# Kernel optimization log

Hardware: AMD Instinct MI355X
Metric: run time of the kernel (lower is better)

Reference implementation:

```python
import jax, jax.numpy as jnp
import numpy as np


def _ln(x, w, b):
    m = x.mean(-1, keepdims=True)
    v = x.var(-1, keepdims=True)
    return (x - m) * jax.lax.rsqrt(v + 1e-5) * w + b


def setup_inputs() -> dict:
    key = jax.random.key(0)
    ks = jax.random.split(key, 12)
    B, Cm, T, D, H = 8, 192, 2048, 512, 1536
    n_fft, hop = 1024, 256
    nF = n_fft // 2 + 1
    s = 0.05
    rn = lambda k, shape: jax.random.normal(k, shape, jnp.float32) * s
    window = (0.5 - 0.5 * jnp.cos(2.0 * jnp.pi * jnp.arange(n_fft, dtype=jnp.float32) / n_fft))
    return dict(
        mel=jax.random.normal(ks[0], (B, Cm, T), jnp.float32),
        embed_w=rn(ks[1], (D, Cm, 7)), embed_b=rn(ks[2], (D,)),
        norm_w=jnp.ones((D,), jnp.float32), norm_b=jnp.zeros((D,), jnp.float32),
        blk_dw_w=rn(ks[3], (8, D, 1, 7)), blk_dw_b=rn(ks[4], (8, D)),
        blk_norm_w=jnp.ones((8, D), jnp.float32), blk_norm_b=jnp.zeros((8, D), jnp.float32),
        blk_pw1_w=rn(ks[5], (8, H, D)), blk_pw1_b=rn(ks[6], (8, H)),
        blk_pw2_w=rn(ks[7], (8, D, H)), blk_pw2_b=rn(ks[8], (8, D)),
        blk_gamma=jnp.full((8, D), 0.1, jnp.float32),
        fnorm_w=jnp.ones((D,), jnp.float32), fnorm_b=jnp.zeros((D,), jnp.float32),
        head_w=rn(ks[9], (2 * nF, D)), head_b=rn(ks[10], (2 * nF,)),
        window=window,
        n_fft=n_fft, hop_length=hop,
    )


def _vocoder(mel, embed_w, embed_b, norm_w, norm_b,
             blk_dw_w, blk_dw_b, blk_norm_w, blk_norm_b,
             blk_pw1_w, blk_pw1_b, blk_pw2_w, blk_pw2_b, blk_gamma,
             fnorm_w, fnorm_b, head_w, head_b, window, n_fft, hop_length):
    D = embed_w.shape[0]
    # embed conv: [B,192,T] -> [B,512,T]
    x = jax.lax.conv_general_dilated(mel, embed_w, (1,), [(3, 3)],
                                     dimension_numbers=('NCH', 'OIH', 'NCH'))
    x = x + embed_b[None, :, None]
    x = _ln(x.transpose(0, 2, 1), norm_w, norm_b).transpose(0, 2, 1)

    def blk(x, p):
        dw, db, nw, nb, w1, b1, w2, b2, g = p
        y = jax.lax.conv_general_dilated(x, dw, (1,), [(3, 3)],
                                         dimension_numbers=('NCH', 'OIH', 'NCH'),
                                         feature_group_count=D)
        y = y + db[None, :, None]
        y = _ln(y.transpose(0, 2, 1), nw, nb)          # [B,T,D]
        y = jax.nn.gelu(jnp.einsum('btc,hc->bth', y, w1) + b1, approximate=False)
        y = jnp.einsum('bth,ch->btc', y, w2) + b2
        return x + (g * y).transpose(0, 2, 1), None

    x, _ = jax.lax.scan(blk, x, (blk_dw_w, blk_dw_b, blk_norm_w, blk_norm_b,
                                 blk_pw1_w, blk_pw1_b, blk_pw2_w, blk_pw2_b, blk_gamma))

    h = _ln(x.transpose(0, 2, 1), fnorm_w, fnorm_b)    # [B,T,D]
    out = jnp.einsum('btc,fc->btf', h, head_w) + head_b  # [B,T,2*nF]
    nF = n_fft // 2 + 1
    mag = jnp.minimum(jnp.exp(out[..., :nF]), 100.0)   # [B,T,nF]
    phase = out[..., nF:]
    S_real = mag * jnp.cos(phase)
    S_imag = mag * jnp.sin(phase)

    # real inverse-DFT basis
    n = jnp.arange(n_fft, dtype=jnp.float32)
    k = jnp.arange(nF, dtype=jnp.float32)
    ang = 2.0 * jnp.pi * n[:, None] * k[None, :] / n_fft
    scale = jnp.full((nF,), 2.0 / n_fft, jnp.float32)
    scale = scale.at[0].set(1.0 / n_fft)
    if n_fft % 2 == 0:
        scale = scale.at[-1].set(1.0 / n_fft)
    cos_b = jnp.cos(ang) * scale[None, :]              # [n_fft, nF]
    sin_b = jnp.sin(ang) * scale[None, :]

    frames = (jnp.einsum('btf,nf->btn', S_real, cos_b)
              - jnp.einsum('btf,nf->btn', S_imag, sin_b))  # [B,T,n_fft]
    frames = frames * window[None, None, :]

    B, T, N = frames.shape
    L = (T - 1) * hop_length + n_fft
    idx = jnp.arange(T)[:, None] * hop_length + jnp.arange(n_fft)[None, :]  # [T,n_fft]
    audio = jnp.zeros((B, L), frames.dtype).at[:, idx].add(frames)
    win_sq = window * window
    win_env = jnp.zeros((L,), frames.dtype).at[idx].add(
        jnp.broadcast_to(win_sq, (T, n_fft)))
    audio = audio / (win_env[None, :] + 1e-11)
    c = n_fft // 2
    return audio[:, c:-c]


def reference(mel, embed_w, embed_b, norm_w, norm_b,
              blk_dw_w, blk_dw_b, blk_norm_w, blk_norm_b,
              blk_pw1_w, blk_pw1_b, blk_pw2_w, blk_pw2_b, blk_gamma,
              fnorm_w, fnorm_b, head_w, head_b, window, n_fft, hop_length):
    return _vocoder(mel, embed_w, embed_b, norm_w, norm_b,
                    blk_dw_w, blk_dw_b, blk_norm_w, blk_norm_b,
                    blk_pw1_w, blk_pw1_b, blk_pw2_w, blk_pw2_b, blk_gamma,
                    fnorm_w, fnorm_b, head_w, head_b, window, n_fft, hop_length)
```

## Files before the change

### kernel.cpp

```cpp
#include <hip/hip_runtime.h>
#include <cmath>

#define B_ 8
#define T_ 2048
#define BT_ 16384
#define D_ 512
#define H_ 1536
#define CM_ 192
#define KE_ 1344
#define TP_ 2054
#define NFFT_ 1024
#define NF_ 513
#define HOP_ 256
#define NO2_ 1026
#define NPAD_ 1152
#define KI_ 1088
#define LOUT_ 524032

typedef _Float16 f16;
typedef f16 f16x8 __attribute__((ext_vector_type(8)));
typedef float f32x4 __attribute__((ext_vector_type(4)));

__device__ __forceinline__ float gelu_f(float v) {
    float u = 0.7978845608028654f * v * (1.0f + 0.044715f * v * v);
    float e = __expf(2.0f * u);
    float t = 1.0f - 2.0f * __builtin_amdgcn_rcpf(e + 1.0f);
    return 0.5f * v * (1.0f + t);
}

__device__ __forceinline__ void gload16(const void* g, void* s) {
    __builtin_amdgcn_global_load_lds((const __attribute__((address_space(1))) void*)g,
                                     (__attribute__((address_space(3))) void*)s, 16, 0, 0);
}


__global__ __launch_bounds__(256) void k_cvt(const float* __restrict__ src,
                                             f16* __restrict__ dst, int n) {
    int i = blockIdx.x * 256 + threadIdx.x;
    if (i < n) dst[i] = (f16)src[i];
}

__global__ __launch_bounds__(256) void k_cvt_head(const float* __restrict__ src,
                                                  f16* __restrict__ dst) {
    int i = blockIdx.x * 256 + threadIdx.x;
    if (i >= NPAD_ * D_) return;
    int row = i >> 9;
    dst[i] = (row < NO2_) ? (f16)src[i] : (f16)0.0f;
}

__global__ __launch_bounds__(256) void k_pad_hb(const float* __restrict__ src,
                                                float* __restrict__ dst) {
    int i = blockIdx.x * 256 + threadIdx.x;
    if (i < NPAD_) dst[i] = (i < NO2_) ? src[i] : 0.0f;
}

__global__ __launch_bounds__(256) void k_cvt_embed(const float* __restrict__ src,
                                                   f16* __restrict__ dst) {
    int i = blockIdx.x * 256 + threadIdx.x;
    if (i >= D_ * KE_) return;
    int d = i / KE_;
    int r2 = i - d * KE_;
    int tap = r2 / CM_;
    int c = r2 - tap * CM_;
    dst[i] = (f16)src[(d * CM_ + c) * 7 + tap];
}

__global__ __launch_bounds__(256) void k_cvtdw(const float* __restrict__ dw,
                                               float* __restrict__ dwT) {
    int i = blockIdx.x * 256 + threadIdx.x;
    if (i >= 8 * 7 * 512) return;
    int bl = i / 3584;
    int rem = i - bl * 3584;
    int k = rem >> 9;
    int d = rem & 511;
    dwT[i] = dw[bl * 3584 + d * 7 + k];
}

__global__ __launch_bounds__(256) void k_melT(const float* __restrict__ mel,
                                              f16* __restrict__ mt) {
    int idx = blockIdx.x * 256 + threadIdx.x;
    if (idx >= B_ * TP_ * 24) return;
    int c8 = idx % 24;
    int rem = idx / 24;
    int tp = rem % TP_;
    int b = rem / TP_;
    int t = tp - 3;
    f16x8 v;
    if (t >= 0 && t < T_) {
        const float* mp = mel + ((size_t)b * CM_ + c8 * 8) * T_ + t;
#pragma unroll
        for (int i = 0; i < 8; ++i) v[i] = (f16)mp[(size_t)i * T_];
    } else {
#pragma unroll
        for (int i = 0; i < 8; ++i) v[i] = (f16)0.0f;
    }
    *(f16x8*)(mt + (size_t)idx * 8) = v;
}

__global__ __launch_bounds__(256) void k_expand(const f16* __restrict__ mt,
                                               f16* __restrict__ A) {
    int g = blockIdx.x * 256 + threadIdx.x;
    if (g >= BT_ * 168) return;
    int bt = g / 168;
    int k8 = g - bt * 168;
    int b = bt >> 11;
    int t = bt & (T_ - 1);
    f16x8 v = *(const f16x8*)(mt + ((size_t)(b * TP_ + t) * CM_) + k8 * 8);
    *(f16x8*)(A + (size_t)bt * KE_ + k8 * 8) = v;
}

__global__ __launch_bounds__(256) void k_build_wmat(f16* __restrict__ wmat) {
    int idx = blockIdx.x * 256 + threadIdx.x;
    if (idx >= NFFT_ * KI_) return;
    int n = idx / KI_;
    int f2 = idx - n * KI_;
    float v = 0.0f;
    if (f2 < NF_) {
        int r = (n * f2) & (NFFT_ - 1);
        float sc = (f2 == 0 || f2 == NF_ - 1) ? (1.0f / NFFT_) : (2.0f / NFFT_);
        v = cospif((float)r * (2.0f / NFFT_)) * sc;
    } else if (f2 < NO2_) {
        int f = f2 - NF_;
        int r = (n * f) & (NFFT_ - 1);
        float sc = (f == 0 || f == NF_ - 1) ? (1.0f / NFFT_) : (2.0f / NFFT_);
        v = -sinpif((float)r * (2.0f / NFFT_)) * sc;
    }
    wmat[idx] = (f16)v;
}

template <bool HOUT>
__global__ __launch_bounds__(64) void k_ln(const float* __restrict__ in,
                                           void* __restrict__ out,
                                           const float* __restrict__ w,
                                           const float* __restrict__ b) {
    int row = blockIdx.x;
    int lane = threadIdx.x;
    const float* p = in + (size_t)row * D_ + lane * 8;
    float4 v0 = *(const float4*)p;
    float4 v1 = *(const float4*)(p + 4);
    float s  = v0.x + v0.y + v0.z + v0.w + v1.x + v1.y + v1.z + v1.w;
    float ss = v0.x * v0.x + v0.y * v0.y + v0.z * v0.z + v0.w * v0.w +
               v1.x * v1.x + v1.y * v1.y + v1.z * v1.z + v1.w * v1.w;
#pragma unroll
    for (int off = 32; off > 0; off >>= 1) {
        s  += __shfl_xor(s, off);
        ss += __shfl_xor(ss, off);
    }
    float mean = s * (1.0f / 512.0f);
    float var  = ss * (1.0f / 512.0f) - mean * mean;
    float rs = rsqrtf(var + 1e-5f);
    const float* wp = w + lane * 8;
    const float* bp = b + lane * 8;
    float4 w0 = *(const float4*)wp, w1 = *(const float4*)(wp + 4);
    float4 b0 = *(const float4*)bp, b1 = *(const float4*)(bp + 4);
    float o[8];
    o[0] = (v0.x - mean) * rs * w0.x + b0.x;
    o[1] = (v0.y - mean) * rs * w0.y + b0.y;
    o[2] = (v0.z - mean) * rs * w0.z + b0.z;
    o[3] = (v0.w - mean) * rs * w0.w + b0.w;
    o[4] = (v1.x - mean) * rs * w1.x + b1.x;
    o[5] = (v1.y - mean) * rs * w1.y + b1.y;
    o[6] = (v1.z - mean) * rs * w1.z + b1.z;
    o[7] = (v1.w - mean) * rs * w1.w + b1.w;
    if constexpr (HOUT) {
        f16x8 h;
#pragma unroll
        for (int i = 0; i < 8; ++i) h[i] = (f16)o[i];
        *(f16x8*)((f16*)out + (size_t)row * D_ + lane * 8) = h;
    } else {
        float* q = (float*)out + (size_t)row * D_ + lane * 8;
        *(float4*)q = make_float4(o[0], o[1], o[2], o[3]);
        *(float4*)(q + 4) = make_float4(o[4], o[5], o[6], o[7]);
    }
}

__global__ __launch_bounds__(256) void k_dwln2(const float* __restrict__ x,
                                               const float* __restrict__ dwT,
                                               const float* __restrict__ db,
                                               const float* __restrict__ nw,
                                               const float* __restrict__ nb,
                                               f16* __restrict__ out) {
    __shared__ float xs[22][512];
    int tid = threadIdx.x;
    int blk = blockIdx.x;
    int b = blk >> 7;
    int t0 = (blk & 127) << 4;
    const float* xb = x + ((size_t)b << 20);
#pragma unroll
    for (int i = 0; i < 11; ++i) {
        int idx = tid + (i << 8);
        int row = idx >> 7;
        int c4 = idx & 127;
        int t = t0 + row - 3;
        float4 v = make_float4(0.f, 0.f, 0.f, 0.f);
        if (t >= 0 && t < T_) v = *(const float4*)(xb + ((size_t)t << 9) + (c4 << 2));
        *(float4*)&xs[row][c4 << 2] = v;
    }
    __syncthreads();

    int o = tid & 63;
    int slot = tid >> 6;
    int d0 = o << 3;
    float acc[4][8];
    {
        float4 b0 = *(const float4*)(db + d0);
        float4 b1 = *(const float4*)(db + d0 + 4);
#pragma unroll
        for (int u = 0; u < 4; ++u) {
            acc[u][0] = b0.x; acc[u][1] = b0.y; acc[u][2] = b0.z; acc[u][3] = b0.w;
            acc[u][4] = b1.x; acc[u][5] = b1.y; acc[u][6] = b1.z; acc[u][7] = b1.w;
        }
    }
#pragma unroll
    for (int k = 0; k < 7; ++k) {
        float w8[8];
        *(float4*)&w8[0] = *(const float4*)(dwT + (k << 9) + d0);
        *(float4*)&w8[4] = *(const float4*)(dwT + (k << 9) + d0 + 4);
#pragma unroll
        for (int u = 0; u < 4; ++u) {
            int row = (slot << 2) + u + k;
            float x8[8];
            *(float4*)&x8[0] = *(const float4*)&xs[row][d0];
            *(float4*)&x8[4] = *(const float4*)&xs[row][d0 + 4];
#pragma unroll
            for (int i = 0; i < 8; ++i) acc[u][i] = fmaf(w8[i], x8[i], acc[u][i]);
        }
    }
    float4 w0 = *(const float4*)(nw + d0), w1 = *(const float4*)(nw + d0 + 4);
    float4 n0 = *(const float4*)(nb + d0), n1 = *(const float4*)(nb + d0 + 4);
    float nwv[8] = {w0.x, w0.y, w0.z, w0.w, w1.x, w1.y, w1.z, w1.w};
    float nbv[8] = {n0.x, n0.y, n0.z, n0.w, n1.x, n1.y, n1.z, n1.w};
#pragma unroll
    for (int u = 0; u < 4; ++u) {
        float s = 0.f, ss = 0.f;
#pragma unroll
        for (int i = 0; i < 8; ++i) { s += acc[u][i]; ss = fmaf(acc[u][i], acc[u][i], ss); }
#pragma unroll
        for (int off = 32; off > 0; off >>= 1) {
            s  += __shfl_xor(s, off);
            ss += __shfl_xor(ss, off);
        }
        float mean = s * (1.0f / 512.0f);
        float var  = ss * (1.0f / 512.0f) - mean * mean;
        float rs = rsqrtf(var + 1e-5f);
        f16x8 h;
#pragma unroll
        for (int i = 0; i < 8; ++i)
            h[i] = (f16)((acc[u][i] - mean) * rs * nwv[i] + nbv[i]);
        int t = t0 + (slot << 2) + u;
        *(f16x8*)(out + (((size_t)(b << 11) + t) << 9) + d0) = h;
    }
}

#define MF(d, a, b) d = __builtin_amdgcn_mfma_f32_16x16x32_f16(a, b, d, 0, 0, 0)

#define TSZ_ 4096

__device__ __forceinline__ void stage32(const f16* __restrict__ g, f16* s,
                                        int K, int kof, int tid) {
    int dr0 = tid >> 3;
    int sl  = tid & 7;
#pragma unroll
    for (int i = 0; i < 2; ++i) {
        int d  = dr0 + (i << 5);
        int gs = sl ^ (d & 7);
        int row = (d << 1) + (gs >> 2);
        int kc  = gs & 3;
        gload16(g + (size_t)row * K + kof + (kc << 3),
                s + (d << 6) + (sl << 3));
    }
}

template <int EPI>
__global__ __launch_bounds__(256, 3) void k_hgemm5(const f16* __restrict__ A,
                                                   const f16* __restrict__ W,
                                                   const float* __restrict__ bias,
                                                   const float* __restrict__ gamma,
                                                   void* __restrict__ C,
                                                   int K, int ldc, int nNt) {
    __shared__ f16 lds[3 * 2 * TSZ_];
    int tid = threadIdx.x;
    int nwg = gridDim.x, bid = blockIdx.x;
    int q = nwg >> 3, r = nwg & 7;
    int xcd = bid & 7, lin = bid >> 3;
    int swz = (xcd < r ? xcd * (q + 1) : r * (q + 1) + (xcd - r) * q) + lin;
    int bm = (swz / nNt) << 7;
    int bn = (swz % nNt) << 7;
    const f16* gA = A + (size_t)bm * K;
    const f16* gW = W + (size_t)bn * K;

    int l = tid & 63;
    int wv = tid >> 6;
    int wm = (wv & 1) << 6;
    int wn = (wv >> 1) << 6;
    int lr = l & 15;
    int lk = l >> 4;
    int lrh = lr >> 1;
    int s0l = ((lr & 1) << 2) | lk;

    int offA[4], offB[4];
#pragma unroll
    for (int i = 0; i < 4; ++i) {
        int dA = (wm >> 1) + i * 8 + lrh;
        offA[i] = (dA << 6) + ((s0l ^ (dA & 7)) << 3);
        int dB = (wn >> 1) + i * 8 + lrh;
        offB[i] = (dB << 6) + ((s0l ^ (dB & 7)) << 3);
    }

    f32x4 acc[4][4];
#pragma unroll
    for (int i = 0; i < 4; ++i)
#pragma unroll
        for (int j = 0; j < 4; ++j) acc[i][j] = {0.f, 0.f, 0.f, 0.f};

    int nk = K >> 5;
    f16* s0 = lds;
    f16* s1 = lds + 2 * TSZ_;
    f16* s2 = lds + 4 * TSZ_;

    stage32(gA, s0, K, 0, tid);        stage32(gW, s0 + TSZ_, K, 0, tid);
    stage32(gA, s1, K, 32, tid);       stage32(gW, s1 + TSZ_, K, 32, tid);
    asm volatile("s_waitcnt vmcnt(4)" ::: "memory");
    __builtin_amdgcn_s_barrier();

    for (int t = 0; t < nk; ++t) {
        bool stg = (t + 2 < nk);
        if (stg) {
            int ko = (t + 2) << 5;
            stage32(gA, s2, K, ko, tid);
            stage32(gW, s2 + TSZ_, K, ko, tid);
        }
        f16x8 af[4], bf[4];
#pragma unroll
        for (int i = 0; i < 4; ++i) af[i] = *(const f16x8*)(s0 + offA[i]);
#pragma unroll
        for (int j = 0; j < 4; ++j) bf[j] = *(const f16x8*)(s0 + TSZ_ + offB[j]);
        __builtin_amdgcn_s_setprio(1);
#pragma unroll
        for (int i = 0; i < 4; ++i)
#pragma unroll
            for (int j = 0; j < 4; ++j) MF(acc[i][j], af[i], bf[j]);
        __builtin_amdgcn_s_setprio(0);
        if (stg)               asm volatile("s_waitcnt vmcnt(4)" ::: "memory");
        else if (t + 1 < nk)   asm volatile("s_waitcnt vmcnt(0)" ::: "memory");
        if (t + 1 < nk) {
            __builtin_amdgcn_s_barrier();
            asm volatile("" ::: "memory");
        }
        f16* tmp = s0; s0 = s1; s1 = s2; s2 = tmp;
    }

    int lk4 = lk << 2;
#pragma unroll
    for (int i = 0; i < 4; ++i) {
#pragma unroll
        for (int rr = 0; rr < 4; ++rr) {
            int row = bm + wm + i * 16 + lk4 + rr;
            size_t moff = (size_t)row * ldc;
#pragma unroll
            for (int j = 0; j < 4; ++j) {
                int col = bn + wn + j * 16 + lr;
                float v = acc[i][j][rr];
                if constexpr (EPI == 0) {
                    ((float*)C)[moff + col] = v + bias[col];
                } else if constexpr (EPI == 1) {
                    ((f16*)C)[moff + col] = (f16)gelu_f(v + bias[col]);
                } else if constexpr (EPI == 2) {
                    ((float*)C)[moff + col] += gamma[col] * (v + bias[col]);
                } else {
                    ((f16*)C)[moff + col] = (f16)(v * bias[col]);
                }
            }
        }
    }
}

#define ASZ_ 8192
#define RSZ_ 12288

__device__ __forceinline__ void stageA256(const f16* __restrict__ g, f16* s,
                                          int K, int kof, int tid) {
    int dr0 = tid >> 3;
    int sl  = tid & 7;
#pragma unroll
    for (int i = 0; i < 4; ++i) {
        int d  = dr0 + (i << 5);
        int gs = sl ^ (d & 7);
        int row = (d << 1) + (gs >> 2);
        int kc  = gs & 3;
        gload16(g + (size_t)row * K + kof + (kc << 3),
                s + (d << 6) + (sl << 3));
    }
}

__device__ __forceinline__ void stageB128(const f16* __restrict__ g, f16* s,
                                          int K, int kof, int tid) {
    int dr0 = tid >> 3;
    int sl  = tid & 7;
#pragma unroll
    for (int i = 0; i < 2; ++i) {
        int d  = dr0 + (i << 5);
        int gs = sl ^ (d & 7);
        int row = (d << 1) + (gs >> 2);
        int kc  = gs & 3;
        gload16(g + (size_t)row * K + kof + (kc << 3),
                s + (d << 6) + (sl << 3));
    }
}

template <int EPI>
__global__ __launch_bounds__(256, 2) void k_hgemm7(const f16* __restrict__ A,
                                                   const f16* __restrict__ W,
                                                   const float* __restrict__ bias,
                                                   const float* __restrict__ gamma,
                                                   void* __restrict__ C,
                                                   int K, int ldc, int nNt) {
    __shared__ f16 lds[3 * RSZ_];
    int tid = threadIdx.x;
    int nwg = gridDim.x, bid = blockIdx.x;
    int q = nwg >> 3, r = nwg & 7;
    int xcd = bid & 7, lin = bid >> 3;
    int swz = (xcd < r ? xcd * (q + 1) : r * (q + 1) + (xcd - r) * q) + lin;
    int bm = (swz / nNt) << 8;
    int bn = (swz % nNt) << 7;
    const f16* gA = A + (size_t)bm * K;
    const f16* gW = W + (size_t)bn * K;

    int l = tid & 63;
    int wv = tid >> 6;
    int wm = (wv & 1) << 7;
    int wn = (wv >> 1) << 6;
    int lr = l & 15;
    int lk = l >> 4;
    int lrh = lr >> 1;
    int s0l = ((lr & 1) << 2) | lk;

    int offA[8], offB[4];
#pragma unroll
    for (int i = 0; i < 8; ++i) {
        int dA = (wm >> 1) + i * 8 + lrh;
        offA[i] = (dA << 6) + ((s0l ^ (dA & 7)) << 3);
    }
#pragma unroll
    for (int j = 0; j < 4; ++j) {
        int dB = (wn >> 1) + j * 8 + lrh;
        offB[j] = (dB << 6) + ((s0l ^ (dB & 7)) << 3);
    }

    f32x4 acc[8][4];
#pragma unroll
    for (int i = 0; i < 8; ++i)
#pragma unroll
        for (int j = 0; j < 4; ++j) acc[i][j] = {0.f, 0.f, 0.f, 0.f};

    int nk = K >> 5;
    f16* s0 = lds;
    f16* s1 = lds + RSZ_;
    f16* s2 = lds + 2 * RSZ_;

    stageA256(gA, s0, K, 0, tid);      stageB128(gW, s0 + ASZ_, K, 0, tid);
    stageA256(gA, s1, K, 32, tid);     stageB128(gW, s1 + ASZ_, K, 32, tid);
    asm volatile("s_waitcnt vmcnt(6)" ::: "memory");
    __builtin_amdgcn_s_barrier();

    for (int t = 0; t < nk; ++t) {
        bool stg = (t + 2 < nk);
        if (stg) {
            int ko = (t + 2) << 5;
            stageA256(gA, s2, K, ko, tid);
            stageB128(gW, s2 + ASZ_, K, ko, tid);
        }
        f16x8 af[8], bf[4];
#pragma unroll
        for (int i = 0; i < 8; ++i) af[i] = *(const f16x8*)(s0 + offA[i]);
#pragma unroll
        for (int j = 0; j < 4; ++j) bf[j] = *(const f16x8*)(s0 + ASZ_ + offB[j]);
        __builtin_amdgcn_s_setprio(1);
#pragma unroll
        for (int i = 0; i < 8; ++i)
#pragma unroll
            for (int j = 0; j < 4; ++j) MF(acc[i][j], af[i], bf[j]);
        __builtin_amdgcn_s_setprio(0);
        if (stg)               asm volatile("s_waitcnt vmcnt(6)" ::: "memory");
        else if (t + 1 < nk)   asm volatile("s_waitcnt vmcnt(0)" ::: "memory");
        if (t + 1 < nk) {
            __builtin_amdgcn_s_barrier();
            asm volatile("" ::: "memory");
        }
        f16* tmp = s0; s0 = s1; s1 = s2; s2 = tmp;
    }

    int lk4 = lk << 2;
#pragma unroll
    for (int i = 0; i < 8; ++i) {
#pragma unroll
        for (int rr = 0; rr < 4; ++rr) {
            int row = bm + wm + i * 16 + lk4 + rr;
            size_t moff = (size_t)row * ldc;
#pragma unroll
            for (int j = 0; j < 4; ++j) {
                int col = bn + wn + j * 16 + lr;
                float v = acc[i][j][rr];
                if constexpr (EPI == 0) {
                    ((float*)C)[moff + col] = v + bias[col];
                } else if constexpr (EPI == 1) {
                    ((f16*)C)[moff + col] = (f16)gelu_f(v + bias[col]);
                } else if constexpr (EPI == 2) {
                    ((float*)C)[moff + col] += gamma[col] * (v + bias[col]);
                } else {
                    ((f16*)C)[moff + col] = (f16)(v * bias[col]);
                }
            }
        }
    }
}

__global__ __launch_bounds__(256) void k_srsi(const float* __restrict__ o,
                                              f16* __restrict__ S) {
    int idx = blockIdx.x * 256 + threadIdx.x;
    if (idx >= BT_ * KI_) return;
    int m = idx / KI_;
    int f2 = idx - m * KI_;
    size_t base = (size_t)m * NPAD_;
    float v = 0.0f;
    if (f2 < NF_) {
        float mag = fminf(__expf(o[base + f2]), 100.0f);
        float sn, cs;
        __sincosf(o[base + NF_ + f2], &sn, &cs);
        v = mag * cs;
    } else if (f2 < NO2_) {
        int f = f2 - NF_;
        float mag = fminf(__expf(o[base + f]), 100.0f);
        float sn, cs;
        __sincosf(o[base + NF_ + f], &sn, &cs);
        v = mag * sn;
    }
    S[idx] = (f16)v;
}

__global__ __launch_bounds__(256) void k_gather(const f16* __restrict__ frames,
                                                const float* __restrict__ win,
                                                float* __restrict__ out) {
    int idx = blockIdx.x * 256 + threadIdx.x;
    int b  = idx / LOUT_;
    int lp = idx - b * LOUT_;
    int l = lp + (NFFT_ / 2);
    int thi = l >> 8;
    if (thi > T_ - 1) thi = T_ - 1;
    int tlo = l - (NFFT_ - 1) + (HOP_ - 1);
    tlo = (tlo < 0) ? 0 : (tlo >> 8);
    float num = 0.0f, den = 0.0f;
    for (int t = tlo; t <= thi; ++t) {
        int n = l - (t << 8);
        float wv = win[n];
        num += (float)frames[((size_t)(b * T_ + t) << 10) + n];
        den = fmaf(wv, wv, den);
    }
    out[idx] = num / (den + 1e-11f);
}

extern "C" void kernel_launch(void* const* d_in, const int* in_sizes, int n_in,
                              void* d_out, int out_size, void* d_ws, size_t ws_size,
                              hipStream_t stream) {
    (void)in_sizes; (void)n_in; (void)out_size; (void)ws_size;
    const float* mel     = (const float*)d_in[0];
    const float* embed_w = (const float*)d_in[1];
    const float* embed_b = (const float*)d_in[2];
    const float* norm_w  = (const float*)d_in[3];
    const float* norm_b  = (const float*)d_in[4];
    const float* bdw = (const float*)d_in[5];
    const float* bdb = (const float*)d_in[6];
    const float* bnw = (const float*)d_in[7];
    const float* bnb = (const float*)d_in[8];
    const float* bw1 = (const float*)d_in[9];
    const float* bb1 = (const float*)d_in[10];
    const float* bw2 = (const float*)d_in[11];
    const float* bb2 = (const float*)d_in[12];
    const float* bg  = (const float*)d_in[13];
    const float* fnw = (const float*)d_in[14];
    const float* fnb = (const float*)d_in[15];
    const float* hw  = (const float*)d_in[16];
    const float* hb  = (const float*)d_in[17];
    const float* win = (const float*)d_in[18];

    char* ws = (char*)d_ws;
    float* xbuf   = (float*)ws;
    f16*   melTp  = (f16*)ws;
    f16*   ybuf_h = (f16*)(ws + 33554432);
    f16*   S_h    = (f16*)ws;
    char* R = ws + 50331648;
    f16*   hbuf_h = (f16*)(R + 33554432);
    f16*   A_h    = (f16*)R;
    float* obuf   = (float*)R;
    f16*   frames_h = (f16*)R;
    char* Wr = ws + 134217728;
    f16*   w1_h   = (f16*)Wr;
    f16*   w2_h   = (f16*)(Wr + 12582912);
    f16*   head_h = (f16*)(Wr + 25165824);
    f16*   wmat_h = (f16*)(Wr + 26345472);
    f16*   we_h   = (f16*)(Wr + 28573696);
    float* hb_pad = (float*)(Wr + 29949952);
    float* dwT    = (float*)(Wr + 29954560);

    const int nW1 = 8 * H_ * D_;
    k_cvt<<<(nW1 + 255) / 256, 256, 0, stream>>>(bw1, w1_h, nW1);
    k_cvt<<<(nW1 + 255) / 256, 256, 0, stream>>>(bw2, w2_h, nW1);
    k_cvt_embed<<<(D_ * KE_ + 255) / 256, 256, 0, stream>>>(embed_w, we_h);
    k_cvt_head<<<(NPAD_ * D_ + 255) / 256, 256, 0, stream>>>(hw, head_h);
    k_pad_hb<<<5, 256, 0, stream>>>(hb, hb_pad);
    k_cvtdw<<<(8 * 3584 + 255) / 256, 256, 0, stream>>>(bdw, dwT);
    k_build_wmat<<<(NFFT_ * KI_ + 255) / 256, 256, 0, stream>>>(wmat_h);

    k_melT<<<(B_ * TP_ * 24 + 255) / 256, 256, 0, stream>>>(mel, melTp);
    k_expand<<<(BT_ * 168 + 255) / 256, 256, 0, stream>>>(melTp, A_h);
    k_hgemm5<0><<<128 * 4, 256, 0, stream>>>(A_h, we_h, embed_b, nullptr, xbuf,
                                             KE_, D_, 4);
    k_ln<false><<<BT_, 64, 0, stream>>>(xbuf, xbuf, norm_w, norm_b);

    for (int bl = 0; bl < 8; ++bl) {
        k_dwln2<<<B_ * 128, 256, 0, stream>>>(xbuf, dwT + bl * 3584, bdb + bl * D_,
                                              bnw + bl * D_, bnb + bl * D_, ybuf_h);
        k_hgemm7<1><<<64 * 12, 256, 0, stream>>>(ybuf_h, w1_h + (size_t)bl * H_ * D_,
                                                 bb1 + bl * H_, nullptr, hbuf_h,
                                                 D_, H_, 12);
        k_hgemm5<2><<<128 * 4, 256, 0, stream>>>(hbuf_h, w2_h + (size_t)bl * D_ * H_,
                                                 bb2 + bl * D_, bg + bl * D_, xbuf,
                                                 H_, D_, 4);
    }

    k_ln<true><<<BT_, 64, 0, stream>>>(xbuf, ybuf_h, fnw, fnb);
    k_hgemm7<0><<<64 * 9, 256, 0, stream>>>(ybuf_h, head_h, hb_pad, nullptr, obuf,
                                            D_, NPAD_, 9);
    k_srsi<<<(BT_ * KI_ + 255) / 256, 256, 0, stream>>>(obuf, S_h);
    k_hgemm7<3><<<64 * 8, 256, 0, stream>>>(S_h, wmat_h, win, nullptr, frames_h,
                                            KI_, NFFT_, 8);
    k_gather<<<B_ * LOUT_ / 256, 256, 0, stream>>>(frames_h, win, (float*)d_out);
}
```

Measured before the change: 1.074 ms.

## Store residual stream in fp16 and switch pw1/head GEMMs to smaller-tile kernel

The residual activation buffer xbuf moves from fp32 to fp16. The embed GEMM, layer norms, depthwise+LN kernel and pw2 residual epilogue now read and write half precision, roughly halving residual-stream memory traffic per block. The pw1 and head GEMMs also move from the 256-row hgemm7 kernel to the 128-row hgemm5 kernel with twice the grid, which changes tiling and occupancy. Accumulating the residual in fp16 across 8 blocks risks accuracy loss.

```diff
diff --git a/kernel.cpp b/kernel.cpp
--- a/kernel.cpp
+++ b/kernel.cpp
@@ -128,19 +128,19 @@
     wmat[idx] = (f16)v;
 }
 
-template <bool HOUT>
-__global__ __launch_bounds__(64) void k_ln(const float* __restrict__ in,
-                                           void* __restrict__ out,
-                                           const float* __restrict__ w,
-                                           const float* __restrict__ b) {
+__global__ __launch_bounds__(64) void k_lnh(const f16* __restrict__ in,
+                                            f16* __restrict__ out,
+                                            const float* __restrict__ w,
+                                            const float* __restrict__ b) {
     int row = blockIdx.x;
     int lane = threadIdx.x;
-    const float* p = in + (size_t)row * D_ + lane * 8;
-    float4 v0 = *(const float4*)p;
-    float4 v1 = *(const float4*)(p + 4);
-    float s  = v0.x + v0.y + v0.z + v0.w + v1.x + v1.y + v1.z + v1.w;
-    float ss = v0.x * v0.x + v0.y * v0.y + v0.z * v0.z + v0.w * v0.w +
-               v1.x * v1.x + v1.y * v1.y + v1.z * v1.z + v1.w * v1.w;
+    f16x8 hv = *(const f16x8*)(in + (size_t)row * D_ + lane * 8);
+    float x[8];
+#pragma unroll
+    for (int i = 0; i < 8; ++i) x[i] = (float)hv[i];
+    float s = 0.f, ss = 0.f;
+#pragma unroll
+    for (int i = 0; i < 8; ++i) { s += x[i]; ss = fmaf(x[i], x[i], ss); }
 #pragma unroll
     for (int off = 32; off > 0; off >>= 1) {
         s  += __shfl_xor(s, off);
@@ -153,48 +153,45 @@
     const float* bp = b + lane * 8;
     float4 w0 = *(const float4*)wp, w1 = *(const float4*)(wp + 4);
     float4 b0 = *(const float4*)bp, b1 = *(const float4*)(bp + 4);
-    float o[8];
-    o[0] = (v0.x - mean) * rs * w0.x + b0.x;
-    o[1] = (v0.y - mean) * rs * w0.y + b0.y;
-    o[2] = (v0.z - mean) * rs * w0.z + b0.z;
-    o[3] = (v0.w - mean) * rs * w0.w + b0.w;
-    o[4] = (v1.x - mean) * rs * w1.x + b1.x;
-    o[5] = (v1.y - mean) * rs * w1.y + b1.y;
-    o[6] = (v1.z - mean) * rs * w1.z + b1.z;
-    o[7] = (v1.w - mean) * rs * w1.w + b1.w;
-    if constexpr (HOUT) {
-        f16x8 h;
-#pragma unroll
-        for (int i = 0; i < 8; ++i) h[i] = (f16)o[i];
-        *(f16x8*)((f16*)out + (size_t)row * D_ + lane * 8) = h;
-    } else {
-        float* q = (float*)out + (size_t)row * D_ + lane * 8;
-        *(float4*)q = make_float4(o[0], o[1], o[2], o[3]);
-        *(float4*)(q + 4) = make_float4(o[4], o[5], o[6], o[7]);
-    }
-}
-
-__global__ __launch_bounds__(256) void k_dwln2(const float* __restrict__ x,
-                                               const float* __restrict__ dwT,
-                                               const float* __restrict__ db,
-                                               const float* __restrict__ nw,
-                                               const float* __restrict__ nb,
-                                               f16* __restrict__ out) {
+    float wv[8] = {w0.x, w0.y, w0.z, w0.w, w1.x, w1.y, w1.z, w1.w};
+    float bv[8] = {b0.x, b0.y, b0.z, b0.w, b1.x, b1.y, b1.z, b1.w};
+    f16x8 h;
+#pragma unroll
+    for (int i = 0; i < 8; ++i) h[i] = (f16)((x[i] - mean) * rs * wv[i] + bv[i]);
+    *(f16x8*)(out + (size_t)row * D_ + lane * 8) = h;
+}
+
+__global__ __launch_bounds__(256) void k_dwln2h(const f16* __restrict__ x,
+                                                const float* __restrict__ dwT,
+                                                const float* __restrict__ db,
+                                                const float* __restrict__ nw,
+                                                const float* __restrict__ nb,
+                                                f16* __restrict__ out) {
     __shared__ float xs[22][512];
     int tid = threadIdx.x;
     int blk = blockIdx.x;
     int b = blk >> 7;
     int t0 = (blk & 127) << 4;
-    const float* xb = x + ((size_t)b << 20);
-#pragma unroll
-    for (int i = 0; i < 11; ++i) {
+    const f16* xb = x + ((size_t)b << 20);
+#pragma unroll
+    for (int i = 0; i < 6; ++i) {
         int idx = tid + (i << 8);
-        int row = idx >> 7;
-        int c4 = idx & 127;
-        int t = t0 + row - 3;
-        float4 v = make_float4(0.f, 0.f, 0.f, 0.f);
-        if (t >= 0 && t < T_) v = *(const float4*)(xb + ((size_t)t << 9) + (c4 << 2));
-        *(float4*)&xs[row][c4 << 2] = v;
+        if (idx < 22 * 64) {
+            int row = idx >> 6;
+            int c8 = idx & 63;
+            int t = t0 + row - 3;
+            float v[8];
+            if (t >= 0 && t < T_) {
+                f16x8 hv = *(const f16x8*)(xb + ((size_t)t << 9) + (c8 << 3));
+#pragma unroll
+                for (int u = 0; u < 8; ++u) v[u] = (float)hv[u];
+            } else {
+#pragma unroll
+                for (int u = 0; u < 8; ++u) v[u] = 0.0f;
+            }
+            *(float4*)&xs[row][c8 << 3] = make_float4(v[0], v[1], v[2], v[3]);
+            *(float4*)&xs[row][(c8 << 3) + 4] = make_float4(v[4], v[5], v[6], v[7]);
+        }
     }
     __syncthreads();
 
@@ -365,8 +362,12 @@
                     ((float*)C)[moff + col] = v + bias[col];
                 } else if constexpr (EPI == 1) {
                     ((f16*)C)[moff + col] = (f16)gelu_f(v + bias[col]);
-                } else if constexpr (EPI == 2) {
-                    ((float*)C)[moff + col] += gamma[col] * (v + bias[col]);
+                } else if constexpr (EPI == 4) {
+                    ((f16*)C)[moff + col] = (f16)(v + bias[col]);
+                } else if constexpr (EPI == 5) {
+                    f16* Cp = (f16*)C;
+                    float old = (float)Cp[moff + col];
+                    Cp[moff + col] = (f16)(old + gamma[col] * (v + bias[col]));
                 } else {
                     ((f16*)C)[moff + col] = (f16)(v * bias[col]);
                 }
@@ -503,10 +504,6 @@
                 float v = acc[i][j][rr];
                 if constexpr (EPI == 0) {
                     ((float*)C)[moff + col] = v + bias[col];
-                } else if constexpr (EPI == 1) {
-                    ((f16*)C)[moff + col] = (f16)gelu_f(v + bias[col]);
-                } else if constexpr (EPI == 2) {
-                    ((float*)C)[moff + col] += gamma[col] * (v + bias[col]);
                 } else {
                     ((f16*)C)[moff + col] = (f16)(v * bias[col]);
                 }
@@ -584,7 +581,7 @@
     const float* win = (const float*)d_in[18];
 
     char* ws = (char*)d_ws;
-    float* xbuf   = (float*)ws;
+    f16*   xbuf_h = (f16*)ws;
     f16*   melTp  = (f16*)ws;
     f16*   ybuf_h = (f16*)(ws + 33554432);
     f16*   S_h    = (f16*)ws;
@@ -613,24 +610,24 @@
 
     k_melT<<<(B_ * TP_ * 24 + 255) / 256, 256, 0, stream>>>(mel, melTp);
     k_expand<<<(BT_ * 168 + 255) / 256, 256, 0, stream>>>(melTp, A_h);
-    k_hgemm5<0><<<128 * 4, 256, 0, stream>>>(A_h, we_h, embed_b, nullptr, xbuf,
+    k_hgemm5<4><<<128 * 4, 256, 0, stream>>>(A_h, we_h, embed_b, nullptr, xbuf_h,
                                              KE_, D_, 4);
-    k_ln<false><<<BT_, 64, 0, stream>>>(xbuf, xbuf, norm_w, norm_b);
+    k_lnh<<<BT_, 64, 0, stream>>>(xbuf_h, xbuf_h, norm_w, norm_b);
 
     for (int bl = 0; bl < 8; ++bl) {
-        k_dwln2<<<B_ * 128, 256, 0, stream>>>(xbuf, dwT + bl * 3584, bdb + bl * D_,
-                                              bnw + bl * D_, bnb + bl * D_, ybuf_h);
-        k_hgemm7<1><<<64 * 12, 256, 0, stream>>>(ybuf_h, w1_h + (size_t)bl * H_ * D_,
-                                                 bb1 + bl * H_, nullptr, hbuf_h,
-                                                 D_, H_, 12);
-        k_hgemm5<2><<<128 * 4, 256, 0, stream>>>(hbuf_h, w2_h + (size_t)bl * D_ * H_,
-                                                 bb2 + bl * D_, bg + bl * D_, xbuf,
+        k_dwln2h<<<B_ * 128, 256, 0, stream>>>(xbuf_h, dwT + bl * 3584, bdb + bl * D_,
+                                               bnw + bl * D_, bnb + bl * D_, ybuf_h);
+        k_hgemm5<1><<<128 * 12, 256, 0, stream>>>(ybuf_h, w1_h + (size_t)bl * H_ * D_,
+                                                  bb1 + bl * H_, nullptr, hbuf_h,
+                                                  D_, H_, 12);
+        k_hgemm5<5><<<128 * 4, 256, 0, stream>>>(hbuf_h, w2_h + (size_t)bl * D_ * H_,
+                                                 bb2 + bl * D_, bg + bl * D_, xbuf_h,
                                                  H_, D_, 4);
     }
 
-    k_ln<true><<<BT_, 64, 0, stream>>>(xbuf, ybuf_h, fnw, fnb);
-    k_hgemm7<0><<<64 * 9, 256, 0, stream>>>(ybuf_h, head_h, hb_pad, nullptr, obuf,
-                                            D_, NPAD_, 9);
+    k_lnh<<<BT_, 64, 0, stream>>>(xbuf_h, ybuf_h, fnw, fnb);
+    k_hgemm5<0><<<128 * 9, 256, 0, stream>>>(ybuf_h, head_h, hb_pad, nullptr, obuf,
+                                             D_, NPAD_, 9);
     k_srsi<<<(BT_ * KI_ + 255) / 256, 256, 0, stream>>>(obuf, S_h);
     k_hgemm7<3><<<64 * 8, 256, 0, stream>>>(S_h, wmat_h, win, nullptr, frames_h,
                                             KI_, NFFT_, 8);
```

New measurement: 986.9 us. 8.1% less time.
